# Optimization experiments

Hardware: AMD Instinct MI355X
Metric: run time of the kernel (lower is better)

Reference implementation:

```python
import jax, jax.numpy as jnp
import numpy as np

N = 200_000        # atoms
E = 800_000        # directed edges (pairs e, e^1 are mutual reverses)
H = 512            # hidden_size
AF = 133           # atom_feat_size
BF = 14            # bond_feat_size
B = 4096           # num graphs


def setup_inputs() -> dict:
    key = jax.random.key(0)
    ks = jax.random.split(key, 8)
    atom_hiddens = jax.random.normal(ks[0], (N, H), dtype=jnp.float32)
    # undirected bonds, then interleave as (src,dst),(dst,src) so rev[e] = e ^ 1
    src = jax.random.randint(ks[1], (E // 2,), 0, N, dtype=jnp.int32)
    dst = jax.random.randint(ks[2], (E // 2,), 0, N, dtype=jnp.int32)
    heads = jnp.stack([src, dst], axis=1).reshape(-1)   # [E]
    tails = jnp.stack([dst, src], axis=1).reshape(-1)   # [E]
    edge_index = jnp.stack([heads, tails], axis=0)      # [2, E]
    rev_edge_index = jnp.arange(E, dtype=jnp.int32) ^ 1
    batch = jnp.sort(jax.random.randint(ks[3], (N,), 0, B, dtype=jnp.int32))
    batch = batch.at[-1].set(B - 1)  # batch[-1]+1 == B, matching the torch code
    s = 1.0 / np.sqrt(H)
    return {
        "atom_hiddens": atom_hiddens,
        "W_node": jax.random.normal(ks[4], (H, AF), dtype=jnp.float32) * s,
        "b_node": jnp.zeros((AF,), dtype=jnp.float32),
        "W_edge": jax.random.normal(ks[5], (H, BF), dtype=jnp.float32) * s,
        "b_edge": jnp.zeros((BF,), dtype=jnp.float32),
        "W_g1": jax.random.normal(ks[6], (H, H), dtype=jnp.float32) * s,
        "b_g1": jnp.zeros((H,), dtype=jnp.float32),
        "W_g2": jax.random.normal(ks[7], (H, 1), dtype=jnp.float32) * s,
        "b_g2": jnp.zeros((1,), dtype=jnp.float32),
        "edge_index": edge_index,
        "rev_edge_index": rev_edge_index,
        "batch": batch,
        "num_graphs": B,
    }


def reference(atom_hiddens, W_node, b_node, W_edge, b_edge, W_g1, b_g1,
              W_g2, b_g2, edge_index, rev_edge_index, batch, num_graphs):
    # graph pooling: index_add_ over the sorted batch vector
    graph_emb = jax.ops.segment_sum(atom_hiddens, batch, num_segments=num_graphs)
    # node head
    node_pred = atom_hiddens @ W_node + b_node
    # edge dedup: the torch loop keeps edge e iff its reverse was not yet
    # visited, i.e. iff e < rev_edge_index[e] (rev is an involution), giving
    # exactly E//2 kept edges.
    e_ids = jnp.arange(edge_index.shape[1])
    keep = jnp.nonzero(e_ids < rev_edge_index, size=edge_index.shape[1] // 2,
                       fill_value=0)[0]
    a1 = edge_index[0, keep]
    a2 = edge_index[1, keep]
    bond_emb = 0.5 * (atom_hiddens[a1] + atom_hiddens[a2])  # [E//2, H]
    edge_pred = bond_emb @ W_edge + b_edge
    # graph head: Linear -> ReLU -> Linear
    graph_pred = jax.nn.relu(graph_emb @ W_g1 + b_g1) @ W_g2 + b_g2
    return node_pred, edge_pred, graph_pred
```

## Files before the change

### kernel.cpp

```cpp
#include <hip/hip_runtime.h>

#define NATOMS 200000
#define NEDGE  800000
#define NBOND  400000
#define HDIM   512
#define AF     133
#define BFEAT  14
#define NGRAPH 4096

#define NODE_OUT_SZ (NATOMS * AF)
#define EDGE_OUT_SZ (NBOND * BFEAT)

#define WS_P     0
#define WS_BMAT  12800000
#define WS_BIAS  12963840
#define WS_GEF   12964480
#define WS_WG1T  21353088

typedef _Float16 half8 __attribute__((ext_vector_type(8)));
typedef float floatx4 __attribute__((ext_vector_type(4)));

__global__ void pack_kernel(const float* __restrict__ Wn, const float* __restrict__ bn,
                            const float* __restrict__ We, const float* __restrict__ be,
                            const float* __restrict__ Wg1, const float* __restrict__ bg2,
                            _Float16* __restrict__ Bmat, float* __restrict__ bias,
                            _Float16* __restrict__ Wg1t, float* __restrict__ gpred) {
    int idx = blockIdx.x * 256 + threadIdx.x;
    if (idx < 160 * 512) {
        int n = idx >> 9, k = idx & 511;
        float v = 0.f;
        if (n < AF)              v = Wn[k * AF + n];
        else if (n < AF + BFEAT) v = We[k * BFEAT + (n - AF)];
        Bmat[idx] = (_Float16)v;
    } else if (idx < 160 * 512 + 512 * 512) {
        int i = idx - 160 * 512;
        int n = i >> 9, k = i & 511;
        Wg1t[i] = (_Float16)Wg1[k * HDIM + n];
    } else if (idx < 160 * 512 + 512 * 512 + 160) {
        int n = idx - (160 * 512 + 512 * 512);
        float v = 0.f;
        if (n < AF)              v = bn[n];
        else if (n < AF + BFEAT) v = be[n - AF];
        bias[n] = v;
    } else if (idx < 160 * 512 + 512 * 512 + 160 + NGRAPH) {
        gpred[idx - (160 * 512 + 512 * 512 + 160)] = bg2[0];
    }
}

__global__ void zero_ge(float4* __restrict__ GEf4) {
    GEf4[blockIdx.x * 256 + threadIdx.x] = make_float4(0.f, 0.f, 0.f, 0.f);
}

__global__ __launch_bounds__(256) void gemm_node(const float* __restrict__ A,
                                                 const _Float16* __restrict__ Bm,
                                                 const float* __restrict__ bias,
                                                 const int* __restrict__ batch,
                                                 float* __restrict__ node_out,
                                                 float* __restrict__ P,
                                                 float* __restrict__ GEf) {
    __shared__ _Float16 As[128][72];
    __shared__ _Float16 Bs[160][72];
    __shared__ int bg[128];

    const int t    = threadIdx.x;
    const int bm   = blockIdx.x;
    const int w    = t >> 6, l = t & 63, quad = l >> 4, lr = l & 15;
    const int wm   = w & 1, wn = w >> 1;

    if (t < 128) {
        int grow = bm * 128 + t;
        bg[t] = (grow < NATOMS) ? batch[grow] : -1;
    }

    floatx4 acc[4][5];
    for (int mt = 0; mt < 4; ++mt)
        for (int nt = 0; nt < 5; ++nt)
            acc[mt][nt] = (floatx4){0.f, 0.f, 0.f, 0.f};

    const int arow0 = t >> 2;
    const int aseg  = (t & 3) * 16;
    const int pc    = t & 63;
    const int pq    = w;

    for (int ko = 0; ko < 8; ++ko) {
        const int k0 = ko * 64;
        float4 av[2][4];
        for (int p = 0; p < 2; ++p) {
            int row = arow0 + p * 64;
            long grow = (long)bm * 128 + row;
            if (grow < NATOMS) {
                const float4* src = (const float4*)(A + grow * HDIM + k0 + aseg);
                av[p][0] = src[0]; av[p][1] = src[1]; av[p][2] = src[2]; av[p][3] = src[3];
            } else {
                av[p][0] = av[p][1] = av[p][2] = av[p][3] = make_float4(0.f, 0.f, 0.f, 0.f);
            }
        }
        uint4 bv[5];
        for (int it = 0; it < 5; ++it) {
            int idx = t + it * 256;
            int row = idx >> 3, c = (idx & 7) * 8;
            bv[it] = *(const uint4*)(Bm + row * HDIM + k0 + c);
        }
        __syncthreads();
        for (int p = 0; p < 2; ++p) {
            int row = arow0 + p * 64;
            half8 h0 = {(_Float16)av[p][0].x, (_Float16)av[p][0].y, (_Float16)av[p][0].z, (_Float16)av[p][0].w,
                        (_Float16)av[p][1].x, (_Float16)av[p][1].y, (_Float16)av[p][1].z, (_Float16)av[p][1].w};
            half8 h1 = {(_Float16)av[p][2].x, (_Float16)av[p][2].y, (_Float16)av[p][2].z, (_Float16)av[p][2].w,
                        (_Float16)av[p][3].x, (_Float16)av[p][3].y, (_Float16)av[p][3].z, (_Float16)av[p][3].w};
            *(half8*)&As[row][aseg]     = h0;
            *(half8*)&As[row][aseg + 8] = h1;
        }
        for (int it = 0; it < 5; ++it) {
            int idx = t + it * 256;
            int row = idx >> 3, c = (idx & 7) * 8;
            *(uint4*)&Bs[row][c] = bv[it];
        }
        __syncthreads();
        for (int kk = 0; kk < 64; kk += 32) {
            half8 af[4], bf[5];
            for (int mt = 0; mt < 4; ++mt)
                af[mt] = *(const half8*)&As[wm * 64 + mt * 16 + lr][kk + quad * 8];
            for (int nt = 0; nt < 5; ++nt)
                bf[nt] = *(const half8*)&Bs[wn * 80 + nt * 16 + lr][kk + quad * 8];
            for (int mt = 0; mt < 4; ++mt)
                for (int nt = 0; nt < 5; ++nt)
                    acc[mt][nt] = __builtin_amdgcn_mfma_f32_16x16x32_f16(af[mt], bf[nt], acc[mt][nt], 0, 0, 0);
        }
        {
            float psum = 0.f;
            int pg = bg[pq * 32];
            for (int r = pq * 32; r < pq * 32 + 32; ++r) {
                int gid = bg[r];
                if (gid != pg) {
                    if (pg >= 0) atomicAdd(&GEf[(size_t)pg * HDIM + k0 + pc], psum);
                    psum = 0.f; pg = gid;
                }
                psum += (float)As[r][pc];
            }
            if (pg >= 0) atomicAdd(&GEf[(size_t)pg * HDIM + k0 + pc], psum);
        }
    }

    float biasv[5];
    for (int nt = 0; nt < 5; ++nt) biasv[nt] = bias[wn * 80 + nt * 16 + lr];
    for (int mt = 0; mt < 4; ++mt) {
        int rbase = bm * 128 + wm * 64 + mt * 16 + quad * 4;
        for (int r = 0; r < 4; ++r) {
            int grow = rbase + r;
            if (grow >= NATOMS) continue;
            for (int nt = 0; nt < 5; ++nt) {
                int gcol = wn * 80 + nt * 16 + lr;
                float v = acc[mt][nt][r] + biasv[nt];
                if (gcol < AF)                  node_out[(long)grow * AF + gcol] = v;
                else if (gcol < AF + BFEAT)     P[(long)grow * 16 + (gcol - AF)] = v;
            }
        }
    }
}

__global__ __launch_bounds__(256) void edge_kernel(const int* __restrict__ ei,
                                                   const float* __restrict__ P,
                                                   float* __restrict__ eout) {
    int t  = threadIdx.x;
    int j  = t & 15, bi = t >> 4;
    int b  = blockIdx.x * 16 + bi;
    if (b >= NBOND) return;
    if (j < BFEAT) {
        int e  = 2 * b;
        int a1 = ei[e];
        int a2 = ei[NEDGE + e];
        float v = 0.5f * (P[(size_t)a1 * 16 + j] + P[(size_t)a2 * 16 + j]);
        eout[(size_t)b * BFEAT + j] = v;
    }
}

__global__ __launch_bounds__(256) void gemm_graph(const float* __restrict__ GEf,
                                                  const _Float16* __restrict__ Bt,
                                                  const float* __restrict__ bg1,
                                                  const float* __restrict__ wg2,
                                                  float* __restrict__ gpred) {
    __shared__ _Float16 As[128][72];
    __shared__ _Float16 Bs[128][72];

    const int t   = threadIdx.x;
    const int bmb = blockIdx.x, bnb = blockIdx.y;
    const int w   = t >> 6, l = t & 63, quad = l >> 4, lr = l & 15;
    const int wm  = w & 1, wn = w >> 1;

    floatx4 acc[4][4];
    for (int mt = 0; mt < 4; ++mt)
        for (int nt = 0; nt < 4; ++nt)
            acc[mt][nt] = (floatx4){0.f, 0.f, 0.f, 0.f};

    const int arow0 = t >> 2;
    const int aseg  = (t & 3) * 16;

    for (int ko = 0; ko < 8; ++ko) {
        const int k0 = ko * 64;
        float4 av[2][4];
        for (int p = 0; p < 2; ++p) {
            int row = bmb * 128 + arow0 + p * 64;
            const float4* src = (const float4*)(GEf + (size_t)row * HDIM + k0 + aseg);
            av[p][0] = src[0]; av[p][1] = src[1]; av[p][2] = src[2]; av[p][3] = src[3];
        }
        uint4 bvv[4];
        for (int it = 0; it < 4; ++it) {
            int idx = t + it * 256;
            int row = idx >> 3, c = (idx & 7) * 8;
            bvv[it] = *(const uint4*)(Bt + (size_t)(bnb * 128 + row) * HDIM + k0 + c);
        }
        __syncthreads();
        for (int p = 0; p < 2; ++p) {
            int row = arow0 + p * 64;
            half8 h0 = {(_Float16)av[p][0].x, (_Float16)av[p][0].y, (_Float16)av[p][0].z, (_Float16)av[p][0].w,
                        (_Float16)av[p][1].x, (_Float16)av[p][1].y, (_Float16)av[p][1].z, (_Float16)av[p][1].w};
            half8 h1 = {(_Float16)av[p][2].x, (_Float16)av[p][2].y, (_Float16)av[p][2].z, (_Float16)av[p][2].w,
                        (_Float16)av[p][3].x, (_Float16)av[p][3].y, (_Float16)av[p][3].z, (_Float16)av[p][3].w};
            *(half8*)&As[row][aseg]     = h0;
            *(half8*)&As[row][aseg + 8] = h1;
        }
        for (int it = 0; it < 4; ++it) {
            int idx = t + it * 256;
            int row = idx >> 3, c = (idx & 7) * 8;
            *(uint4*)&Bs[row][c] = bvv[it];
        }
        __syncthreads();
        for (int kk = 0; kk < 64; kk += 32) {
            half8 af[4], bf[4];
            for (int mt = 0; mt < 4; ++mt)
                af[mt] = *(const half8*)&As[wm * 64 + mt * 16 + lr][kk + quad * 8];
            for (int nt = 0; nt < 4; ++nt)
                bf[nt] = *(const half8*)&Bs[wn * 64 + nt * 16 + lr][kk + quad * 8];
            for (int mt = 0; mt < 4; ++mt)
                for (int nt = 0; nt < 4; ++nt)
                    acc[mt][nt] = __builtin_amdgcn_mfma_f32_16x16x32_f16(af[mt], bf[nt], acc[mt][nt], 0, 0, 0);
        }
    }

    float bg1v[4], wg2v[4];
    for (int nt = 0; nt < 4; ++nt) {
        int col = bnb * 128 + wn * 64 + nt * 16 + lr;
        bg1v[nt] = bg1[col];
        wg2v[nt] = wg2[col];
    }
    for (int mt = 0; mt < 4; ++mt) {
        for (int r = 0; r < 4; ++r) {
            int row = bmb * 128 + wm * 64 + mt * 16 + quad * 4 + r;
            float partial = 0.f;
            for (int nt = 0; nt < 4; ++nt) {
                float v = acc[mt][nt][r] + bg1v[nt];
                v = v > 0.f ? v : 0.f;
                partial += v * wg2v[nt];
            }
            partial += __shfl_xor(partial, 1);
            partial += __shfl_xor(partial, 2);
            partial += __shfl_xor(partial, 4);
            partial += __shfl_xor(partial, 8);
            if (lr == 0) atomicAdd(&gpred[row], partial);
        }
    }
}

extern "C" void kernel_launch(void* const* d_in, const int* in_sizes, int n_in,
                              void* d_out, int out_size, void* d_ws, size_t ws_size,
                              hipStream_t stream) {
    const float* A    = (const float*)d_in[0];
    const float* Wn   = (const float*)d_in[1];
    const float* bn   = (const float*)d_in[2];
    const float* We   = (const float*)d_in[3];
    const float* be   = (const float*)d_in[4];
    const float* Wg1  = (const float*)d_in[5];
    const float* bg1  = (const float*)d_in[6];
    const float* Wg2  = (const float*)d_in[7];
    const float* bg2  = (const float*)d_in[8];
    const int*   ei   = (const int*)d_in[9];
    const int*   batch= (const int*)d_in[11];

    char* ws = (char*)d_ws;
    float*    P    = (float*)(ws + WS_P);
    _Float16* Bmat = (_Float16*)(ws + WS_BMAT);
    float*    bias = (float*)(ws + WS_BIAS);
    float*    GEf  = (float*)(ws + WS_GEF);
    _Float16* Wg1t = (_Float16*)(ws + WS_WG1T);

    float* node_out = (float*)d_out;
    float* edge_out = node_out + NODE_OUT_SZ;
    float* gpred    = edge_out + EDGE_OUT_SZ;

    pack_kernel<<<dim3(1361), dim3(256), 0, stream>>>(Wn, bn, We, be, Wg1, bg2, Bmat, bias, Wg1t, gpred);
    zero_ge<<<dim3(NGRAPH * HDIM / 4 / 256), dim3(256), 0, stream>>>((float4*)GEf);
    gemm_node<<<dim3((NATOMS + 127) / 128), dim3(256), 0, stream>>>(A, Bmat, bias, batch, node_out, P, GEf);
    edge_kernel<<<dim3(NBOND / 16), dim3(256), 0, stream>>>(ei, P, edge_out);
    gemm_graph<<<dim3(32, 4), dim3(256), 0, stream>>>(GEf, Wg1t, bg1, Wg2, gpred);
}
```

Measured before the change: 746.4 us.

## Use direct global-to-LDS B loads, swizzle Bs, and stage node output for coalesced stores

B tiles now go straight from global memory into a swizzled LDS layout via global_load_lds, so they no longer pass through registers. The B fragment reads use an XOR swizzle to avoid bank conflicts. Pooling reads batch ids by wavefront shuffle instead of from LDS, and it batches the LDS reads of As rows. The node_pred epilogue stages 64-row tiles in LDS (unioned with the GEMM buffers) and writes them out as contiguous float4 stores, replacing the scattered 133-stride scalar stores. The cost is extra syncs and a bounds risk: the float4 copy of a partial last tile assumes every row exists, though 200000 divides evenly by 64.

Result: no change. 750.6 us (+0.5%).

```diff
diff --git a/kernel.cpp b/kernel.cpp
--- a/kernel.cpp
+++ b/kernel.cpp
@@ -19,6 +19,9 @@
 
 typedef _Float16 half8 __attribute__((ext_vector_type(8)));
 typedef float floatx4 __attribute__((ext_vector_type(4)));
+
+#define GLOBAL_CV(p) ((const __attribute__((address_space(1))) void*)(p))
+#define LDS_V(p)     ((__attribute__((address_space(3))) void*)(p))
 
 __global__ void pack_kernel(const float* __restrict__ Wn, const float* __restrict__ bn,
                             const float* __restrict__ We, const float* __restrict__ be,
@@ -58,8 +61,13 @@
                                                  float* __restrict__ node_out,
                                                  float* __restrict__ P,
                                                  float* __restrict__ GEf) {
-    __shared__ _Float16 As[128][72];
-    __shared__ _Float16 Bs[160][72];
+    __shared__ union {
+        struct {
+            _Float16 As[128][72];
+            _Float16 Bs[160 * 64];
+        } k;
+        float stage[64 * 133];
+    } sm;
     __shared__ int bg[128];
 
     const int t    = threadIdx.x;
@@ -79,8 +87,13 @@
 
     const int arow0 = t >> 2;
     const int aseg  = (t & 3) * 16;
-    const int pc    = t & 63;
-    const int pq    = w;
+    const int pc    = l;
+
+    int bgl;
+    {
+        __syncthreads();
+        bgl = bg[w * 32 + (l & 31)];
+    }
 
     for (int ko = 0; ko < 8; ++ko) {
         const int k0 = ko * 64;
@@ -95,48 +108,57 @@
                 av[p][0] = av[p][1] = av[p][2] = av[p][3] = make_float4(0.f, 0.f, 0.f, 0.f);
             }
         }
-        uint4 bv[5];
+        __syncthreads();
         for (int it = 0; it < 5; ++it) {
             int idx = t + it * 256;
-            int row = idx >> 3, c = (idx & 7) * 8;
-            bv[it] = *(const uint4*)(Bm + row * HDIM + k0 + c);
-        }
-        __syncthreads();
+            int row = idx >> 3;
+            int c8  = (idx & 7) ^ (row & 7);
+            const _Float16* src = Bm + row * HDIM + k0 + c8 * 8;
+            char* ldsbase = (char*)&sm.k.Bs[0] + ((w * 64) + it * 256) * 16;
+            __builtin_amdgcn_global_load_lds(GLOBAL_CV(src), LDS_V(ldsbase), 16, 0, 0);
+        }
         for (int p = 0; p < 2; ++p) {
             int row = arow0 + p * 64;
             half8 h0 = {(_Float16)av[p][0].x, (_Float16)av[p][0].y, (_Float16)av[p][0].z, (_Float16)av[p][0].w,
                         (_Float16)av[p][1].x, (_Float16)av[p][1].y, (_Float16)av[p][1].z, (_Float16)av[p][1].w};
             half8 h1 = {(_Float16)av[p][2].x, (_Float16)av[p][2].y, (_Float16)av[p][2].z, (_Float16)av[p][2].w,
                         (_Float16)av[p][3].x, (_Float16)av[p][3].y, (_Float16)av[p][3].z, (_Float16)av[p][3].w};
-            *(half8*)&As[row][aseg]     = h0;
-            *(half8*)&As[row][aseg + 8] = h1;
-        }
-        for (int it = 0; it < 5; ++it) {
-            int idx = t + it * 256;
-            int row = idx >> 3, c = (idx & 7) * 8;
-            *(uint4*)&Bs[row][c] = bv[it];
+            *(half8*)&sm.k.As[row][aseg]     = h0;
+            *(half8*)&sm.k.As[row][aseg + 8] = h1;
         }
         __syncthreads();
         for (int kk = 0; kk < 64; kk += 32) {
             half8 af[4], bf[5];
             for (int mt = 0; mt < 4; ++mt)
-                af[mt] = *(const half8*)&As[wm * 64 + mt * 16 + lr][kk + quad * 8];
-            for (int nt = 0; nt < 5; ++nt)
-                bf[nt] = *(const half8*)&Bs[wn * 80 + nt * 16 + lr][kk + quad * 8];
+                af[mt] = *(const half8*)&sm.k.As[wm * 64 + mt * 16 + lr][kk + quad * 8];
+            for (int nt = 0; nt < 5; ++nt) {
+                int row = wn * 80 + nt * 16 + lr;
+                int c8  = (quad + (kk >> 3)) ^ (row & 7);
+                bf[nt] = *(const half8*)&sm.k.Bs[(row * 8 + c8) * 8];
+            }
             for (int mt = 0; mt < 4; ++mt)
                 for (int nt = 0; nt < 5; ++nt)
                     acc[mt][nt] = __builtin_amdgcn_mfma_f32_16x16x32_f16(af[mt], bf[nt], acc[mt][nt], 0, 0, 0);
         }
         {
+            const int rbase = w * 32;
             float psum = 0.f;
-            int pg = bg[pq * 32];
-            for (int r = pq * 32; r < pq * 32 + 32; ++r) {
-                int gid = bg[r];
-                if (gid != pg) {
-                    if (pg >= 0) atomicAdd(&GEf[(size_t)pg * HDIM + k0 + pc], psum);
-                    psum = 0.f; pg = gid;
+            int pg = __shfl(bgl, 0);
+            float rv[16];
+            #pragma unroll
+            for (int h = 0; h < 2; ++h) {
+                #pragma unroll
+                for (int i = 0; i < 16; ++i)
+                    rv[i] = (float)sm.k.As[rbase + h * 16 + i][pc];
+                #pragma unroll
+                for (int i = 0; i < 16; ++i) {
+                    int gid = __shfl(bgl, h * 16 + i);
+                    if (gid != pg) {
+                        if (pg >= 0) atomicAdd(&GEf[(size_t)pg * HDIM + k0 + pc], psum);
+                        psum = 0.f; pg = gid;
+                    }
+                    psum += rv[i];
                 }
-                psum += (float)As[r][pc];
             }
             if (pg >= 0) atomicAdd(&GEf[(size_t)pg * HDIM + k0 + pc], psum);
         }
@@ -144,16 +166,41 @@
 
     float biasv[5];
     for (int nt = 0; nt < 5; ++nt) biasv[nt] = bias[wn * 80 + nt * 16 + lr];
+
     for (int mt = 0; mt < 4; ++mt) {
-        int rbase = bm * 128 + wm * 64 + mt * 16 + quad * 4;
+        int rbase0 = bm * 128 + wm * 64 + mt * 16 + quad * 4;
         for (int r = 0; r < 4; ++r) {
-            int grow = rbase + r;
+            int grow = rbase0 + r;
             if (grow >= NATOMS) continue;
             for (int nt = 0; nt < 5; ++nt) {
                 int gcol = wn * 80 + nt * 16 + lr;
-                float v = acc[mt][nt][r] + biasv[nt];
-                if (gcol < AF)                  node_out[(long)grow * AF + gcol] = v;
-                else if (gcol < AF + BFEAT)     P[(long)grow * 16 + (gcol - AF)] = v;
+                if (gcol >= AF && gcol < AF + BFEAT)
+                    P[(long)grow * 16 + (gcol - AF)] = acc[mt][nt][r] + biasv[nt];
+            }
+        }
+    }
+
+    for (int phase = 0; phase < 2; ++phase) {
+        long rowbase = (long)bm * 128 + phase * 64;
+        __syncthreads();
+        if (wm == phase) {
+            for (int mt = 0; mt < 4; ++mt) {
+                for (int r = 0; r < 4; ++r) {
+                    int rl = mt * 16 + quad * 4 + r;
+                    for (int nt = 0; nt < 5; ++nt) {
+                        int gcol = wn * 80 + nt * 16 + lr;
+                        if (gcol < AF)
+                            sm.stage[rl * 133 + gcol] = acc[mt][nt][r] + biasv[nt];
+                    }
+                }
+            }
+        }
+        __syncthreads();
+        if (rowbase < NATOMS) {
+            float* dst = node_out + rowbase * AF;
+            for (int i = t; i < (64 * 133) / 4; i += 256) {
+                float4 v = *(const float4*)&sm.stage[i * 4];
+                *(float4*)&dst[i * 4] = v;
             }
         }
     }
```
